# Performance work log

Hardware: AMD Instinct MI355X
Metric: run time of the kernel (lower is better)

Reference implementation:

```python
import jax, jax.numpy as jnp
import numpy as np

B, N_OBS = 4096, 64
H = 256
SCALE = 0.05  # keep activations stable through SQUARE/MUL layers


def setup_inputs() -> dict:
    key = jax.random.key(0)
    ks = jax.random.split(key, 16)
    rn = lambda k, shp, s=SCALE: s * jax.random.normal(k, shp, dtype=jnp.float32)
    return {
        "x": jax.random.normal(ks[0], (B, N_OBS), dtype=jnp.float32),
        "xdot": jax.random.normal(ks[1], (B, N_OBS), dtype=jnp.float32),
        "w1": rn(ks[2], (H, N_OBS)), "b1": rn(ks[3], (H,)),
        "w2a": rn(ks[4], (H, H)), "b2a": rn(ks[5], (H,)),
        "w2b": rn(ks[6], (H, H)), "b2b": rn(ks[7], (H,)),
        "w3a": rn(ks[8], (H, H)), "b3a": rn(ks[9], (H,)),
        "w3s": rn(ks[10], (H, N_OBS)), "b3s": rn(ks[11], (H,)),
        "wout": rn(ks[12], (1, H)),
        "scalar": jax.random.normal(ks[13], (1,), dtype=jnp.float32),
    }


def reference(x, xdot, w1, b1, w2a, b2a, w2b, b2b, w3a, b3a, w3s, b3s, wout, scalar):
    # mul path: empty mul_activation -> yy = x*0 + scalar  (shape [B, n_obs])
    yy = x * 0 + scalar

    # Layer 1: SQUARE. Initial jac is identity, so
    # matmul(2*diag(z), W1) @ I == 2*z[:,:,None] * W1
    z = x @ w1.T + b1                      # [B, H]
    y = z * z
    jac = (2.0 * z)[:, :, None] * w1[None]  # [B, H, N_OBS]

    # Layer 2: MUL. diag(z1)@W2b + diag(z2)@W2a == z1[:,:,None]*w2b + z2[:,:,None]*w2a
    z1 = y @ w2a.T + b2a
    z2 = y @ w2b.T + b2b
    y = z1 * z2
    grad = z1[:, :, None] * w2b[None] + z2[:, :, None] * w2a[None]  # [B, H, H]
    jac = jnp.einsum('boh,bhi->boi', grad, jac)                      # [B, H, N_OBS]

    # Layer 3: SKIP. jac = diag(z1)@W3s + (diag(z2)@W3a)@jac
    z1 = y @ w3a.T + b3a
    z2 = x @ w3s.T + b3s
    y = z1 * z2
    jac = z1[:, :, None] * w3s[None] + z2[:, :, None] * jnp.einsum('oh,bhi->boi', w3a, jac)

    numerical_b = y @ wout.T                                # [B, 1]
    jac = jnp.einsum('oh,bhi->boi', wout, jac)              # [B, 1, N_OBS]
    numerical_bdot = jnp.sum(jac[:, 0, :] * xdot, axis=1)   # [B]
    return (numerical_b, numerical_bdot, y, yy)
```

## Files before the change

### kernel.cpp

```cpp
#include <hip/hip_runtime.h>

typedef unsigned short ushort_t;
typedef unsigned int uint_t;
typedef __bf16 bf16x8 __attribute__((ext_vector_type(8)));
typedef float f32x4 __attribute__((ext_vector_type(4)));

#define H 256
#define RPB 16
#define NBLK 256

#define NB_OFF 0
#define BDOT_OFF 4096
#define Y_OFF 8192
#define YY_OFF (8192 + 4096 * 256)

__device__ __forceinline__ ushort_t f2bf(float x) {
    union { float f; uint_t u; } c; c.f = x;
    uint_t r = (c.u + 0x7FFFu + ((c.u >> 16) & 1u)) >> 16;
    return (ushort_t)r;
}
__device__ __forceinline__ float bf2f(ushort_t v) {
    union { uint_t u; float f; } c; c.u = ((uint_t)v) << 16;
    return c.f;
}

#define O_W1b  0
#define O_W1T  16384
#define O_W2ab 32768
#define O_W2bb 98304
#define O_W3ab 163840
#define O_W2aT 229376
#define O_W2bT 294912
#define O_W3aT 360448
#define O_W3sb 425984
#define O_W3sT 442368

__global__ __launch_bounds__(256) void prep_weights(
    const float* __restrict__ w1, const float* __restrict__ w2a,
    const float* __restrict__ w2b, const float* __restrict__ w3a,
    const float* __restrict__ w3s, const float* __restrict__ wout,
    ushort_t* __restrict__ ws) {
    __shared__ float tile[64][65];
    int b = blockIdx.x;
    const float* src; int Oo, Ot, R, C, t; bool scl;
    if (b < 16)      { src = w2a; Oo = O_W2ab; Ot = O_W2aT; R = 256; C = 256; t = b;      scl = false; }
    else if (b < 32) { src = w2b; Oo = O_W2bb; Ot = O_W2bT; R = 256; C = 256; t = b - 16; scl = false; }
    else if (b < 48) { src = w3a; Oo = O_W3ab; Ot = O_W3aT; R = 256; C = 256; t = b - 32; scl = true;  }
    else if (b < 52) { src = w1;  Oo = O_W1b;  Ot = O_W1T;  R = 256; C = 64;  t = b - 48; scl = false; }
    else             { src = w3s; Oo = O_W3sb; Ot = O_W3sT; R = 256; C = 64;  t = b - 52; scl = true;  }
    int tr, tc;
    if (C == 256) { tr = t >> 2; tc = t & 3; } else { tr = t; tc = 0; }
    int r0 = tr * 64, c0 = tc * 64;

    union pack8 { ushort_t u[8]; uint4 q; };
    for (int it = threadIdx.x; it < 512; it += 256) {
        int r = it >> 3, c8 = (it & 7) << 3;
        const float* s = src + (r0 + r) * C + c0 + c8;
        pack8 p;
#pragma unroll
        for (int j = 0; j < 8; j++) { float v = s[j]; tile[r][c8 + j] = v; p.u[j] = f2bf(v); }
        *(uint4*)(ws + Oo + (r0 + r) * C + c0 + c8) = p.q;
    }
    __syncthreads();
    for (int it = threadIdx.x; it < 512; it += 256) {
        int cc = it >> 3, r8 = (it & 7) << 3;
        pack8 p;
#pragma unroll
        for (int j = 0; j < 8; j++) {
            float v = tile[r8 + j][cc];
            if (scl) v *= wout[r0 + r8 + j];
            p.u[j] = f2bf(v);
        }
        *(uint4*)(ws + Ot + (c0 + cc) * R + r0 + r8) = p.q;
    }
}

#define U_BA   0
#define U_BB   16384
#define U_X    32768
#define U_Z    33792
#define U_Y    37888
#define U_Z12  41984
#define U_Z22  46080
#define U_Z13  50176
#define U_Z23  54272
#define U_U    58368
#define U_XD   62464
#define U_NB   66560
#define SMEM_USHORTS 66624
#define SMEM_BYTES (SMEM_USHORTS * 2)

__device__ __forceinline__ void gload16(const ushort_t* g, ushort_t* l) {
    __builtin_amdgcn_global_load_lds(
        (const __attribute__((address_space(1))) void*)g,
        (__attribute__((address_space(3))) void*)l, 16, 0, 0);
}

__device__ __forceinline__ int posw(int r, int c) { return r * H + (c ^ ((r & 7) << 3)); }

template <bool SUM>
__device__ __forceinline__ void staged_dual(
    const ushort_t* __restrict__ g0, const ushort_t* __restrict__ g1,
    const ushort_t* sA0, const ushort_t* sA1,
    ushort_t* sB0, ushort_t* sB1,
    int wid, int lane, f32x4& acc0, f32x4& acc1) {
    const int nsrc = (wid << 4) + (lane >> 2);
    const int osrc = ((lane & 3) ^ (nsrc & 3)) << 3;
    const ushort_t* s0 = g0 + nsrc * 256 + osrc;
    const ushort_t* s1 = g1 + nsrc * 256 + osrc;
    const int dstb = wid << 9;
    const int row = lane & 15;
    const int nn = (wid << 4) + row;
    const int kq = (lane >> 4) << 3;
    const int boff = nn * 32 + (kq ^ ((nn & 3) << 3));
    const int sw = (row & 7) << 3;
    const ushort_t* a0p = sA0 + row * 256;
    const ushort_t* a1p = sA1 + row * 256;

    gload16(s0, sB0 + dstb);
    gload16(s1, sB1 + dstb);
#pragma unroll
    for (int c = 0; c < 8; ++c) {
        if (c < 7) {
            int nb = ((c + 1) & 1) << 13;
            gload16(s0 + (c + 1) * 32, sB0 + nb + dstb);
            gload16(s1 + (c + 1) * 32, sB1 + nb + dstb);
            asm volatile("s_waitcnt vmcnt(2)" ::: "memory");
        } else {
            asm volatile("s_waitcnt vmcnt(0)" ::: "memory");
        }
        __builtin_amdgcn_s_barrier();
        __builtin_amdgcn_sched_barrier(0);
        int cb = (c & 1) << 13;
        bf16x8 a0 = *(const bf16x8*)(a0p + (((c << 5) + kq) ^ sw));
        bf16x8 b0 = *(const bf16x8*)(sB0 + cb + boff);
        bf16x8 a1 = *(const bf16x8*)(a1p + (((c << 5) + kq) ^ sw));
        bf16x8 b1 = *(const bf16x8*)(sB1 + cb + boff);
        acc0 = __builtin_amdgcn_mfma_f32_16x16x32_bf16(a0, b0, acc0, 0, 0, 0);
        if (SUM)
            acc0 = __builtin_amdgcn_mfma_f32_16x16x32_bf16(a1, b1, acc0, 0, 0, 0);
        else
            acc1 = __builtin_amdgcn_mfma_f32_16x16x32_bf16(a1, b1, acc1, 0, 0, 0);
        __builtin_amdgcn_sched_barrier(0);
        __builtin_amdgcn_s_barrier();
    }
}

template <int NF, int STRA, int STRB>
__device__ __forceinline__ void gemm_one(const ushort_t* sA, const ushort_t* __restrict__ B0,
                                         int lane, int k0, f32x4& acc0) {
    const int row = lane & 15;
    const int kq = (lane >> 4) << 3;
    const int sw = (row & 7) << 3;
    bf16x8 b0[NF], a[NF];
    const ushort_t* bp0 = B0 + row * STRB + k0 + kq;
    const ushort_t* ap = sA + row * STRA;
#pragma unroll
    for (int i = 0; i < NF; i++) b0[i] = *(const bf16x8*)(bp0 + i * 32);
#pragma unroll
    for (int i = 0; i < NF; i++) a[i] = *(const bf16x8*)(ap + ((k0 + i * 32 + kq) ^ sw));
    __builtin_amdgcn_sched_barrier(0);
#pragma unroll
    for (int i = 0; i < NF; i++)
        acc0 = __builtin_amdgcn_mfma_f32_16x16x32_bf16(a[i], b0[i], acc0, 0, 0, 0);
}

__global__ __launch_bounds__(1024) void net_main(
    const float* __restrict__ x, const float* __restrict__ xd,
    const float* __restrict__ b1, const float* __restrict__ b2a,
    const float* __restrict__ b2b, const float* __restrict__ b3a,
    const float* __restrict__ b3s, const float* __restrict__ wout,
    const float* __restrict__ scalar, const ushort_t* __restrict__ ws,
    float* __restrict__ out) {
    extern __shared__ __align__(16) ushort_t smem[];
    ushort_t* sBA = smem + U_BA;
    ushort_t* sBB = smem + U_BB;
    ushort_t* sX  = smem + U_X;
    ushort_t* sZ  = smem + U_Z;
    ushort_t* sY  = smem + U_Y;
    ushort_t* sZ12 = smem + U_Z12;
    ushort_t* sZ22 = smem + U_Z22;
    ushort_t* sZ13 = smem + U_Z13;
    ushort_t* sZ23 = smem + U_Z23;
    ushort_t* sU  = smem + U_U;
    float* sXd = (float*)(smem + U_XD);
    float* sNB = (float*)(smem + U_NB);

    const int tid = threadIdx.x;
    const int wid = tid >> 6;
    const int lane = tid & 63;
    const int row16 = lane & 15;
    const int rq = lane >> 4;
    const int R0 = blockIdx.x * RPB;
    const int n0 = wid * 16;
    const int row = lane & 15;
    const int kq = (lane >> 4) << 3;
    const int sw = (row & 7) << 3;

    bf16x8 pb0, pb1, pb2, pb3;
    {
        const ushort_t* w1p = ws + O_W1b + (n0 + row) * 64 + kq;
        const ushort_t* w3p = ws + O_W3sb + (n0 + row) * 64 + kq;
        pb0 = *(const bf16x8*)(w1p);
        pb1 = *(const bf16x8*)(w1p + 32);
        pb2 = *(const bf16x8*)(w3p);
        pb3 = *(const bf16x8*)(w3p + 32);
    }
    float sc = scalar[0];
    {
        int r = tid >> 6, c = tid & 63;
        sX[r * 64 + (c ^ ((r & 7) << 3))] = f2bf(x[(R0 + r) * 64 + c]);
        sXd[tid] = xd[(R0 + r) * 64 + c];
        out[YY_OFF + (R0 + r) * 64 + c] = sc;
    }
    if (tid < RPB) sNB[tid] = 0.f;
    __syncthreads();

    {
        bf16x8 af0 = *(const bf16x8*)(sX + row * 64 + (kq ^ sw));
        bf16x8 af1 = *(const bf16x8*)(sX + row * 64 + ((32 + kq) ^ sw));
        f32x4 z = {0.f,0.f,0.f,0.f}, q = {0.f,0.f,0.f,0.f};
        z = __builtin_amdgcn_mfma_f32_16x16x32_bf16(af0, pb0, z, 0, 0, 0);
        z = __builtin_amdgcn_mfma_f32_16x16x32_bf16(af1, pb1, z, 0, 0, 0);
        q = __builtin_amdgcn_mfma_f32_16x16x32_bf16(af0, pb2, q, 0, 0, 0);
        q = __builtin_amdgcn_mfma_f32_16x16x32_bf16(af1, pb3, q, 0, 0, 0);
        int c = n0 + row16;
        float bz = b1[c], bs = b3s[c];
#pragma unroll
        for (int i = 0; i < 4; i++) {
            int r = rq * 4 + i;
            int p = posw(r, c);
            float za = z[i] + bz;
            sZ[p] = f2bf(za);
            sY[p] = f2bf(za * za);
            sZ23[p] = f2bf(q[i] + bs);
        }
    }
    __syncthreads();

    {
        f32x4 aA = {0.f,0.f,0.f,0.f}, aB = {0.f,0.f,0.f,0.f};
        staged_dual<false>(ws + O_W2ab, ws + O_W2bb, sY, sY, sBA, sBB, wid, lane, aA, aB);
        int c = n0 + row16;
        float ba = b2a[c], bb = b2b[c];
#pragma unroll
        for (int i = 0; i < 4; i++) {
            int r = rq * 4 + i;
            int p = posw(r, c);
            float z12 = aA[i] + ba, z22 = aB[i] + bb;
            sZ12[p] = f2bf(z12);
            sZ22[p] = f2bf(z22);
            sU[p] = f2bf(z12 * z22);
        }
    }
    __syncthreads();

    {
        f32x4 zz = {0.f,0.f,0.f,0.f}, tt = {0.f,0.f,0.f,0.f};
        staged_dual<false>(ws + O_W3ab, ws + O_W3aT, sU, sZ23, sBA, sBB, wid, lane, zz, tt);
        int c = n0 + row16;
        float ba = b3a[c], wo = wout[c];
#pragma unroll
        for (int i = 0; i < 4; i++) {
            int r = rq * 4 + i;
            int p = posw(r, c);
            float z13 = zz[i] + ba;
            float z23 = bf2f(sZ23[p]);
            float y3 = z13 * z23;
            out[Y_OFF + (R0 + r) * H + c] = y3;
            sZ13[p] = f2bf(z13);
            float t = tt[i];
            sZ12[p] = f2bf(t * bf2f(sZ12[p]));
            sZ22[p] = f2bf(t * bf2f(sZ22[p]));
            float v = wo * y3;
            v += __shfl_xor(v, 1);
            v += __shfl_xor(v, 2);
            v += __shfl_xor(v, 4);
            v += __shfl_xor(v, 8);
            if (row16 == 0) atomicAdd(&sNB[r], v);
        }
    }
    __syncthreads();

    {
        f32x4 pp = {0.f,0.f,0.f,0.f}, dummy = {0.f,0.f,0.f,0.f};
        staged_dual<true>(ws + O_W2bT, ws + O_W2aT, sZ12, sZ22, sBA, sBB, wid, lane, pp, dummy);
        int c = n0 + row16;
#pragma unroll
        for (int i = 0; i < 4; i++) {
            int r = rq * 4 + i;
            int p = posw(r, c);
            sZ[p] = f2bf(2.f * pp[i] * bf2f(sZ[p]));
        }
    }
    __syncthreads();

    {
        int mat = wid >> 3, kh = (wid >> 2) & 1, nt = wid & 3;
        const ushort_t* A = mat ? sZ : sZ13;
        const ushort_t* B = ws + (mat ? O_W1T : O_W3sT) + nt * 16 * H;
        f32x4 acc = {0.f,0.f,0.f,0.f};
        gemm_one<4, H, H>(A, B, lane, kh * 128, acc);
        float* dst = mat ? ((float*)sU + kh * 1024) : ((float*)sY + kh * 1024);
        int c = nt * 16 + row16;
#pragma unroll
        for (int i = 0; i < 4; i++) dst[(rq * 4 + i) * 64 + c] = acc[i];
    }
    __syncthreads();

    {
        float* F0 = (float*)sY;
        float* F1 = F0 + 1024;
        float* F2 = (float*)sU;
        float* F3 = F2 + 1024;
        int r = tid >> 6, j = tid & 63;
        int e = r * 64 + j;
        float s = (F0[e] + F1[e] + F2[e] + F3[e]) * sXd[e];
        s += __shfl_xor(s, 1);
        s += __shfl_xor(s, 2);
        s += __shfl_xor(s, 4);
        s += __shfl_xor(s, 8);
        s += __shfl_xor(s, 16);
        s += __shfl_xor(s, 32);
        if (j == 0) out[BDOT_OFF + R0 + r] = s;
        if (tid < RPB) out[NB_OFF + R0 + tid] = sNB[tid];
    }
}

extern "C" void kernel_launch(void* const* d_in, const int* in_sizes, int n_in,
                              void* d_out, int out_size, void* d_ws, size_t ws_size,
                              hipStream_t stream) {
    (void)in_sizes; (void)n_in; (void)out_size; (void)ws_size;
    const float* x = (const float*)d_in[0];
    const float* xd = (const float*)d_in[1];
    const float* w1 = (const float*)d_in[2];
    const float* b1 = (const float*)d_in[3];
    const float* w2a = (const float*)d_in[4];
    const float* b2a = (const float*)d_in[5];
    const float* w2b = (const float*)d_in[6];
    const float* b2b = (const float*)d_in[7];
    const float* w3a = (const float*)d_in[8];
    const float* b3a = (const float*)d_in[9];
    const float* w3s = (const float*)d_in[10];
    const float* b3s = (const float*)d_in[11];
    const float* wout = (const float*)d_in[12];
    const float* scalar = (const float*)d_in[13];
    ushort_t* ws = (ushort_t*)d_ws;
    float* out = (float*)d_out;

    static bool attr_set = false;
    if (!attr_set) {
        hipFuncSetAttribute((const void*)net_main,
                            hipFuncAttributeMaxDynamicSharedMemorySize, SMEM_BYTES);
        attr_set = true;
    }

    prep_weights<<<56, 256, 0, stream>>>(w1, w2a, w2b, w3a, w3s, wout, ws);
    net_main<<<NBLK, 1024, SMEM_BYTES, stream>>>(x, xd, b1, b2a, b2b, b3a, b3s, wout, scalar, ws, out);
}
```

Before: 33.29 us.

## Drop block barriers in staged weight pipeline, prefetch two ahead, load x directly

Each wave in the staged dual GEMM only reads the weight rows it loaded into LDS itself. So the per-step block-wide s_barriers are removed, and global-to-LDS loads are issued two chunks ahead into the double buffer, after an lgkmcnt wait that keeps the buffer from being overwritten while still in use. The layer-1 input x is now loaded from global memory straight into MFMA operand registers, which drops the sX LDS staging and one __syncthreads. The weight-prep kernel is split into twice as many smaller tiles (112 blocks of 32 rows) for more parallelism. This relies on the per-wave ownership of B rows staying intact, and the x loads become uncoalesced per-lane float4 reads.

```diff
diff --git a/kernel.cpp b/kernel.cpp
--- a/kernel.cpp
+++ b/kernel.cpp
@@ -40,21 +40,22 @@
     const float* __restrict__ w2b, const float* __restrict__ w3a,
     const float* __restrict__ w3s, const float* __restrict__ wout,
     ushort_t* __restrict__ ws) {
-    __shared__ float tile[64][65];
+    __shared__ float tile[32][65];
     int b = blockIdx.x;
-    const float* src; int Oo, Ot, R, C, t; bool scl;
-    if (b < 16)      { src = w2a; Oo = O_W2ab; Ot = O_W2aT; R = 256; C = 256; t = b;      scl = false; }
-    else if (b < 32) { src = w2b; Oo = O_W2bb; Ot = O_W2bT; R = 256; C = 256; t = b - 16; scl = false; }
-    else if (b < 48) { src = w3a; Oo = O_W3ab; Ot = O_W3aT; R = 256; C = 256; t = b - 32; scl = true;  }
-    else if (b < 52) { src = w1;  Oo = O_W1b;  Ot = O_W1T;  R = 256; C = 64;  t = b - 48; scl = false; }
-    else             { src = w3s; Oo = O_W3sb; Ot = O_W3sT; R = 256; C = 64;  t = b - 52; scl = true;  }
+    const float* src; int Oo, Ot, C, t; bool scl;
+    if (b < 32)       { src = w2a; Oo = O_W2ab; Ot = O_W2aT; C = 256; t = b;       scl = false; }
+    else if (b < 64)  { src = w2b; Oo = O_W2bb; Ot = O_W2bT; C = 256; t = b - 32;  scl = false; }
+    else if (b < 96)  { src = w3a; Oo = O_W3ab; Ot = O_W3aT; C = 256; t = b - 64;  scl = true;  }
+    else if (b < 104) { src = w1;  Oo = O_W1b;  Ot = O_W1T;  C = 64;  t = b - 96;  scl = false; }
+    else              { src = w3s; Oo = O_W3sb; Ot = O_W3sT; C = 64;  t = b - 104; scl = true;  }
     int tr, tc;
     if (C == 256) { tr = t >> 2; tc = t & 3; } else { tr = t; tc = 0; }
-    int r0 = tr * 64, c0 = tc * 64;
+    int r0 = tr * 32, c0 = tc * 64;
+    const int tid = threadIdx.x;
 
     union pack8 { ushort_t u[8]; uint4 q; };
-    for (int it = threadIdx.x; it < 512; it += 256) {
-        int r = it >> 3, c8 = (it & 7) << 3;
+    {
+        int r = tid >> 3, c8 = (tid & 7) << 3;
         const float* s = src + (r0 + r) * C + c0 + c8;
         pack8 p;
 #pragma unroll
@@ -62,8 +63,8 @@
         *(uint4*)(ws + Oo + (r0 + r) * C + c0 + c8) = p.q;
     }
     __syncthreads();
-    for (int it = threadIdx.x; it < 512; it += 256) {
-        int cc = it >> 3, r8 = (it & 7) << 3;
+    {
+        int cc = tid >> 2, r8 = (tid & 3) << 3;
         pack8 p;
 #pragma unroll
         for (int j = 0; j < 8; j++) {
@@ -71,23 +72,22 @@
             if (scl) v *= wout[r0 + r8 + j];
             p.u[j] = f2bf(v);
         }
-        *(uint4*)(ws + Ot + (c0 + cc) * R + r0 + r8) = p.q;
+        *(uint4*)(ws + Ot + (c0 + cc) * 256 + r0 + r8) = p.q;
     }
 }
 
 #define U_BA   0
 #define U_BB   16384
-#define U_X    32768
-#define U_Z    33792
-#define U_Y    37888
-#define U_Z12  41984
-#define U_Z22  46080
-#define U_Z13  50176
-#define U_Z23  54272
-#define U_U    58368
-#define U_XD   62464
-#define U_NB   66560
-#define SMEM_USHORTS 66624
+#define U_Z    32768
+#define U_Y    36864
+#define U_Z12  40960
+#define U_Z22  45056
+#define U_Z13  49152
+#define U_Z23  53248
+#define U_U    57344
+#define U_XD   61440
+#define U_NB   63488
+#define SMEM_USHORTS 63520
 #define SMEM_BYTES (SMEM_USHORTS * 2)
 
 __device__ __forceinline__ void gload16(const ushort_t* g, ushort_t* l) {
@@ -117,32 +117,30 @@
     const ushort_t* a0p = sA0 + row * 256;
     const ushort_t* a1p = sA1 + row * 256;
 
+    asm volatile("s_waitcnt vmcnt(0)" ::: "memory");
     gload16(s0, sB0 + dstb);
     gload16(s1, sB1 + dstb);
+    gload16(s0 + 32, sB0 + 8192 + dstb);
+    gload16(s1 + 32, sB1 + 8192 + dstb);
 #pragma unroll
     for (int c = 0; c < 8; ++c) {
-        if (c < 7) {
-            int nb = ((c + 1) & 1) << 13;
-            gload16(s0 + (c + 1) * 32, sB0 + nb + dstb);
-            gload16(s1 + (c + 1) * 32, sB1 + nb + dstb);
-            asm volatile("s_waitcnt vmcnt(2)" ::: "memory");
-        } else {
-            asm volatile("s_waitcnt vmcnt(0)" ::: "memory");
-        }
-        __builtin_amdgcn_s_barrier();
-        __builtin_amdgcn_sched_barrier(0);
-        int cb = (c & 1) << 13;
+        if (c < 7) asm volatile("s_waitcnt vmcnt(2)" ::: "memory");
+        else       asm volatile("s_waitcnt vmcnt(0)" ::: "memory");
+        const int cb = (c & 1) << 13;
         bf16x8 a0 = *(const bf16x8*)(a0p + (((c << 5) + kq) ^ sw));
         bf16x8 b0 = *(const bf16x8*)(sB0 + cb + boff);
         bf16x8 a1 = *(const bf16x8*)(a1p + (((c << 5) + kq) ^ sw));
         bf16x8 b1 = *(const bf16x8*)(sB1 + cb + boff);
+        if (c < 6) {
+            asm volatile("s_waitcnt lgkmcnt(0)" ::: "memory");
+            gload16(s0 + (c + 2) * 32, sB0 + cb + dstb);
+            gload16(s1 + (c + 2) * 32, sB1 + cb + dstb);
+        }
         acc0 = __builtin_amdgcn_mfma_f32_16x16x32_bf16(a0, b0, acc0, 0, 0, 0);
         if (SUM)
             acc0 = __builtin_amdgcn_mfma_f32_16x16x32_bf16(a1, b1, acc0, 0, 0, 0);
         else
             acc1 = __builtin_amdgcn_mfma_f32_16x16x32_bf16(a1, b1, acc1, 0, 0, 0);
-        __builtin_amdgcn_sched_barrier(0);
-        __builtin_amdgcn_s_barrier();
     }
 }
 
@@ -175,7 +173,6 @@
     extern __shared__ __align__(16) ushort_t smem[];
     ushort_t* sBA = smem + U_BA;
     ushort_t* sBB = smem + U_BB;
-    ushort_t* sX  = smem + U_X;
     ushort_t* sZ  = smem + U_Z;
     ushort_t* sY  = smem + U_Y;
     ushort_t* sZ12 = smem + U_Z12;
@@ -197,33 +194,38 @@
     const int kq = (lane >> 4) << 3;
     const int sw = (row & 7) << 3;
 
-    bf16x8 pb0, pb1, pb2, pb3;
     {
         const ushort_t* w1p = ws + O_W1b + (n0 + row) * 64 + kq;
         const ushort_t* w3p = ws + O_W3sb + (n0 + row) * 64 + kq;
-        pb0 = *(const bf16x8*)(w1p);
-        pb1 = *(const bf16x8*)(w1p + 32);
-        pb2 = *(const bf16x8*)(w3p);
-        pb3 = *(const bf16x8*)(w3p + 32);
-    }
-    float sc = scalar[0];
-    {
-        int r = tid >> 6, c = tid & 63;
-        sX[r * 64 + (c ^ ((r & 7) << 3))] = f2bf(x[(R0 + r) * 64 + c]);
-        sXd[tid] = xd[(R0 + r) * 64 + c];
-        out[YY_OFF + (R0 + r) * 64 + c] = sc;
-    }
-    if (tid < RPB) sNB[tid] = 0.f;
-    __syncthreads();
-
-    {
-        bf16x8 af0 = *(const bf16x8*)(sX + row * 64 + (kq ^ sw));
-        bf16x8 af1 = *(const bf16x8*)(sX + row * 64 + ((32 + kq) ^ sw));
+        bf16x8 pb0 = *(const bf16x8*)(w1p);
+        bf16x8 pb1 = *(const bf16x8*)(w1p + 32);
+        bf16x8 pb2 = *(const bf16x8*)(w3p);
+        bf16x8 pb3 = *(const bf16x8*)(w3p + 32);
+        const float* xg = x + (R0 + row) * 64;
+        float4 x0 = *(const float4*)(xg + kq);
+        float4 x1 = *(const float4*)(xg + kq + 4);
+        float4 x2 = *(const float4*)(xg + 32 + kq);
+        float4 x3 = *(const float4*)(xg + 32 + kq + 4);
+        float sc = scalar[0];
+        {
+            int r = tid >> 6, c = tid & 63;
+            sXd[tid] = xd[(R0 + r) * 64 + c];
+            out[YY_OFF + (R0 + r) * 64 + c] = sc;
+            if (tid < RPB) sNB[tid] = 0.f;
+        }
+        union { ushort_t u[8]; bf16x8 v; } A0, A1;
+#pragma unroll
+        for (int j = 0; j < 4; j++) {
+            A0.u[j]     = f2bf(((const float*)&x0)[j]);
+            A0.u[4 + j] = f2bf(((const float*)&x1)[j]);
+            A1.u[j]     = f2bf(((const float*)&x2)[j]);
+            A1.u[4 + j] = f2bf(((const float*)&x3)[j]);
+        }
         f32x4 z = {0.f,0.f,0.f,0.f}, q = {0.f,0.f,0.f,0.f};
-        z = __builtin_amdgcn_mfma_f32_16x16x32_bf16(af0, pb0, z, 0, 0, 0);
-        z = __builtin_amdgcn_mfma_f32_16x16x32_bf16(af1, pb1, z, 0, 0, 0);
-        q = __builtin_amdgcn_mfma_f32_16x16x32_bf16(af0, pb2, q, 0, 0, 0);
-        q = __builtin_amdgcn_mfma_f32_16x16x32_bf16(af1, pb3, q, 0, 0, 0);
+        z = __builtin_amdgcn_mfma_f32_16x16x32_bf16(A0.v, pb0, z, 0, 0, 0);
+        z = __builtin_amdgcn_mfma_f32_16x16x32_bf16(A1.v, pb1, z, 0, 0, 0);
+        q = __builtin_amdgcn_mfma_f32_16x16x32_bf16(A0.v, pb2, q, 0, 0, 0);
+        q = __builtin_amdgcn_mfma_f32_16x16x32_bf16(A1.v, pb3, q, 0, 0, 0);
         int c = n0 + row16;
         float bz = b1[c], bs = b3s[c];
 #pragma unroll
@@ -355,6 +357,6 @@
         attr_set = true;
     }
 
-    prep_weights<<<56, 256, 0, stream>>>(w1, w2a, w2b, w3a, w3s, wout, ws);
+    prep_weights<<<112, 256, 0, stream>>>(w1, w2a, w2b, w3a, w3s, wout, ws);
     net_main<<<NBLK, 1024, SMEM_BYTES, stream>>>(x, xd, b1, b2a, b2b, b3a, b3s, wout, scalar, ws, out);
 }
```

Result: faster. 30.51 us (-8.3%).
